# Kernel tuning notes

Hardware: AMD Instinct MI355X
Metric: run time of the kernel (lower is better)

Reference implementation:

```python
import jax, jax.numpy as jnp
import numpy as np

B, H, W, C = 16, 64, 64, 512
C2 = C // 2
LN_EPS = 1e-3  # Keras LayerNormalization default epsilon


def setup_inputs() -> dict:
    key = jax.random.key(0)
    ks = jax.random.split(key, 8)
    s = 0.02
    return {
        "x": jax.random.normal(ks[0], (B, H, W, C), dtype=jnp.float32),
        "ch_wv_w": jax.random.normal(ks[1], (C, C2), dtype=jnp.float32) * s,
        "ch_wv_b": jnp.zeros((C2,), jnp.float32),
        "ch_wq_w": jax.random.normal(ks[2], (C, 1), dtype=jnp.float32) * s,
        "ch_wq_b": jnp.zeros((1,), jnp.float32),
        "ch_wz_w": jax.random.normal(ks[3], (C2, C), dtype=jnp.float32) * s,
        "ch_wz_b": jnp.zeros((C,), jnp.float32),
        "ln_gamma": jnp.ones((C,), jnp.float32),
        "ln_beta": jnp.zeros((C,), jnp.float32),
        "sp_wv_w": jax.random.normal(ks[4], (C, C2), dtype=jnp.float32) * s,
        "sp_wv_b": jnp.zeros((C2,), jnp.float32),
        "sp_wq_w": jax.random.normal(ks[5], (C, C2), dtype=jnp.float32) * s,
        "sp_wq_b": jnp.zeros((C2,), jnp.float32),
    }


def reference(x, ch_wv_w, ch_wv_b, ch_wq_w, ch_wq_b, ch_wz_w, ch_wz_b,
              ln_gamma, ln_beta, sp_wv_w, sp_wv_b, sp_wq_w, sp_wq_b):
    b, h, w, c = x.shape
    n = h * w
    c2 = c // 2

    # ---- channel-only branch ----
    # 1x1 convs are pointwise GEMMs over the channel dim
    ch_wv = jnp.einsum('bhwc,cd->bhwd', x, ch_wv_w) + ch_wv_b      # (B,H,W,C/2)
    ch_wq = jnp.einsum('bhwc,co->bhwo', x, ch_wq_w) + ch_wq_b      # (B,H,W,1)
    ch_wv = ch_wv.reshape(b, n, c2)                                # (B,N,C/2)
    ch_wq = jax.nn.softmax(ch_wq.reshape(b, n, 1), axis=1)         # softmax over N
    ch_wz = jnp.einsum('bnd,bno->bd', ch_wv, ch_wq)                # (B,C/2)
    ch_wz = jnp.einsum('bd,dc->bc', ch_wz, ch_wz_w) + ch_wz_b      # (B,C)

    # LayerNorm over axes [1,2,3] of (B,1,1,C) == normalize over C
    mean = jnp.mean(ch_wz, axis=-1, keepdims=True)
    var = jnp.var(ch_wz, axis=-1, keepdims=True)
    ch_wz = (ch_wz - mean) * jax.lax.rsqrt(var + LN_EPS) * ln_gamma + ln_beta
    channel_weight = jax.nn.sigmoid(ch_wz)[:, None, None, :]       # (B,1,1,C)
    channel_out = channel_weight * x                               # (B,H,W,C)

    # ---- spatial-only branch ----
    sp_wv = jnp.einsum('bhwc,cd->bhwd', channel_out, sp_wv_w) + sp_wv_b  # (B,H,W,C/2)
    sp_wq = jnp.einsum('bhwc,cd->bhwd', channel_out, sp_wq_w) + sp_wq_b  # (B,H,W,C/2)
    sp_wq = jnp.mean(sp_wq, axis=(1, 2))                           # GAP -> (B,C/2)
    sp_wq = jax.nn.softmax(sp_wq, axis=-1)                         # softmax over C/2
    sp_wv = sp_wv.reshape(b, n, c2)                                # (B,N,C/2)
    sp_wz = jnp.einsum('bd,bnd->bn', sp_wq, sp_wv)                 # (B,N)
    spatial_weight = jax.nn.sigmoid(sp_wz).reshape(b, h, w, 1)     # (B,H,W,1)
    return spatial_weight * channel_out
```

## Files before the change

kernel.cpp:

```cpp
#include <hip/hip_runtime.h>
#include <math.h>

#define BB 16
#define NN 4096
#define CC 512
#define C2 256
#define CHUNKS 32
#define RPC (NN/CHUNKS)

__device__ __forceinline__ float sigmoidf_(float z){ return 1.0f/(1.0f + __expf(-z)); }
__device__ __forceinline__ float dot8_(float4 a0, float4 a1, float4 b0, float4 b1){
    return a0.x*b0.x + a0.y*b0.y + a0.z*b0.z + a0.w*b0.w
         + a1.x*b1.x + a1.y*b1.y + a1.z*b1.z + a1.w*b1.w;
}

__global__ __launch_bounds__(256) void k_stats(const float* __restrict__ x,
        const float* __restrict__ wq,
        float* __restrict__ part_w, float* __restrict__ part_g,
        float* __restrict__ chunk_m, float* __restrict__ chunk_d)
{
    const int b = blockIdx.x / CHUNKS;
    const int k = blockIdx.x % CHUNKS;
    const int tid = threadIdx.x, lane = tid & 63, wv = tid >> 6;
    __shared__ float s_log[RPC];
    __shared__ float s_e[RPC];
    __shared__ float g_part[4][CC];
    const long base = ((long)b*NN + (long)k*RPC) * CC;

    float4 w0 = *(const float4*)(wq + lane*4);
    float4 w1 = *(const float4*)(wq + 256 + lane*4);
    float g0x=0,g0y=0,g0z=0,g0w=0, g1x=0,g1y=0,g1z=0,g1w=0;

    for (int i = 0; i < RPC/4; ++i) {
        const int r = wv*(RPC/4) + i;
        const float* xr = x + base + (long)r*CC;
        float4 a0 = *(const float4*)(xr + lane*4);
        float4 a1 = *(const float4*)(xr + 256 + lane*4);
        float d = dot8_(a0, a1, w0, w1);
        #pragma unroll
        for (int off = 32; off; off >>= 1) d += __shfl_xor(d, off);
        if (lane == 0) s_log[r] = d;
        g0x+=a0.x; g0y+=a0.y; g0z+=a0.z; g0w+=a0.w;
        g1x+=a1.x; g1y+=a1.y; g1z+=a1.z; g1w+=a1.w;
    }
    g_part[wv][lane*4+0]=g0x; g_part[wv][lane*4+1]=g0y;
    g_part[wv][lane*4+2]=g0z; g_part[wv][lane*4+3]=g0w;
    g_part[wv][256+lane*4+0]=g1x; g_part[wv][256+lane*4+1]=g1y;
    g_part[wv][256+lane*4+2]=g1z; g_part[wv][256+lane*4+3]=g1w;
    __syncthreads();

    float m = -3.4e38f;
    #pragma unroll
    for (int r = 0; r < RPC; ++r) m = fmaxf(m, s_log[r]);
    if (tid < RPC) s_e[tid] = __expf(s_log[tid] - m);
    __syncthreads();
    if (tid == 0) {
        float dsum = 0.f;
        for (int r = 0; r < RPC; ++r) dsum += s_e[r];
        chunk_d[b*CHUNKS + k] = dsum;
        chunk_m[b*CHUNKS + k] = m;
    }

    const int c = 2*tid;
    float2 acc = {0.f, 0.f};
    for (int r = 0; r < RPC; ++r) {
        float2 v = *(const float2*)(x + base + (long)r*CC + c);
        float e = s_e[r];
        acc.x = fmaf(e, v.x, acc.x);
        acc.y = fmaf(e, v.y, acc.y);
    }
    *(float2*)(part_w + (long)(b*CHUNKS + k)*CC + c) = acc;
    float2 g;
    g.x = g_part[0][c]   + g_part[1][c]   + g_part[2][c]   + g_part[3][c];
    g.y = g_part[0][c+1] + g_part[1][c+1] + g_part[2][c+1] + g_part[3][c+1];
    *(float2*)(part_g + (long)(b*CHUNKS + k)*CC + c) = g;
}

__global__ __launch_bounds__(256) void k_combine(const float* __restrict__ part_w,
        const float* __restrict__ part_g,
        const float* __restrict__ chunk_m, const float* __restrict__ chunk_d,
        float* __restrict__ xbar, float* __restrict__ gapx)
{
    const int b  = blockIdx.x >> 3;
    const int cs = blockIdx.x & 7;
    const int tid = threadIdx.x, cl = tid & 63, q = tid >> 6;
    const int c = cs*64 + cl;
    __shared__ float s_scale[CHUNKS];
    __shared__ float s_w[4][64];
    __shared__ float s_g[4][64];
    const float* cm = chunk_m + b*CHUNKS;
    const float* cd = chunk_d + b*CHUNKS;
    float m = -3.4e38f;
    #pragma unroll
    for (int k = 0; k < CHUNKS; ++k) m = fmaxf(m, cm[k]);
    if (tid < CHUNKS) s_scale[tid] = __expf(cm[tid] - m);
    __syncthreads();
    float denom = 0.f;
    #pragma unroll
    for (int k = 0; k < CHUNKS; ++k) denom = fmaf(s_scale[k], cd[k], denom);
    float pw = 0.f, pg = 0.f;
    for (int k = q*8; k < q*8+8; ++k) {
        pw = fmaf(s_scale[k], part_w[(long)(b*CHUNKS + k)*CC + c], pw);
        pg += part_g[(long)(b*CHUNKS + k)*CC + c];
    }
    s_w[q][cl] = pw; s_g[q][cl] = pg;
    __syncthreads();
    if (q == 0) {
        float sw_ = s_w[0][cl]+s_w[1][cl]+s_w[2][cl]+s_w[3][cl];
        float sg_ = s_g[0][cl]+s_g[1][cl]+s_g[2][cl]+s_g[3][cl];
        xbar[b*CC + c] = sw_ / denom;
        gapx[b*CC + c] = sg_;
    }
}

__global__ __launch_bounds__(256) void k_gemv_cd(const float* __restrict__ vec,
        const float* __restrict__ W, const float* __restrict__ bias,
        float* __restrict__ out)
{
    const int bx = blockIdx.x;
    const int b  = blockIdx.y;
    const int tid = threadIdx.x, dl = tid & 63, q = tid >> 6;
    const int d = bx*64 + dl;
    __shared__ float s_x[CC];
    __shared__ float s_p[4][64];
    s_x[tid]       = vec[b*CC + tid];
    s_x[tid + 256] = vec[b*CC + tid + 256];
    __syncthreads();
    float a0=0,a1=0,a2=0,a3=0;
    #pragma unroll 8
    for (int c = q*128; c < q*128 + 128; c += 4) {
        a0 = fmaf(s_x[c+0], W[(c+0)*C2 + d], a0);
        a1 = fmaf(s_x[c+1], W[(c+1)*C2 + d], a1);
        a2 = fmaf(s_x[c+2], W[(c+2)*C2 + d], a2);
        a3 = fmaf(s_x[c+3], W[(c+3)*C2 + d], a3);
    }
    s_p[q][dl] = (a0+a1)+(a2+a3);
    __syncthreads();
    if (q == 0)
        out[b*C2 + d] = s_p[0][dl]+s_p[1][dl]+s_p[2][dl]+s_p[3][dl] + bias[d];
}

__global__ __launch_bounds__(256) void k_g2p(const float* __restrict__ mid,
        const float* __restrict__ Wz, float* __restrict__ part2)
{
    const int jd = blockIdx.x;
    const int b  = blockIdx.y;
    const int tid = threadIdx.x;
    __shared__ float s_m[32];
    if (tid < 32) s_m[tid] = mid[b*C2 + jd*32 + tid];
    __syncthreads();
    float a0 = 0.f, a1 = 0.f;
    #pragma unroll 8
    for (int dd = 0; dd < 32; ++dd) {
        const float mm = s_m[dd];
        const int d = jd*32 + dd;
        a0 = fmaf(mm, Wz[d*CC + tid],       a0);
        a1 = fmaf(mm, Wz[d*CC + tid + 256], a1);
    }
    part2[(long)(b*8 + jd)*CC + tid]       = a0;
    part2[(long)(b*8 + jd)*CC + tid + 256] = a1;
}

__global__ __launch_bounds__(256) void k_g2ln(const float* __restrict__ part2,
        const float* __restrict__ bz, const float* __restrict__ ln_g,
        const float* __restrict__ ln_b, const float* __restrict__ gapx,
        float* __restrict__ cw, float* __restrict__ gco)
{
    const int b = blockIdx.x, tid = threadIdx.x, lane = tid & 63, w = tid >> 6;
    __shared__ float s_red[8];
    float z0 = bz[tid], z1 = bz[tid + 256];
    #pragma unroll
    for (int jd = 0; jd < 8; ++jd) {
        z0 += part2[(long)(b*8 + jd)*CC + tid];
        z1 += part2[(long)(b*8 + jd)*CC + tid + 256];
    }
    float sum = z0 + z1, sq = z0*z0 + z1*z1;
    #pragma unroll
    for (int off = 32; off; off >>= 1) { sum += __shfl_xor(sum, off); sq += __shfl_xor(sq, off); }
    if (lane == 0) { s_red[w] = sum; s_red[4 + w] = sq; }
    __syncthreads();
    sum = s_red[0] + s_red[1] + s_red[2] + s_red[3];
    sq  = s_red[4] + s_red[5] + s_red[6] + s_red[7];
    const float mean = sum * (1.f/CC);
    const float var  = sq  * (1.f/CC) - mean*mean;
    const float rstd = rsqrtf(var + 1e-3f);
    float cw0 = sigmoidf_((z0 - mean)*rstd*ln_g[tid]       + ln_b[tid]);
    float cw1 = sigmoidf_((z1 - mean)*rstd*ln_g[tid + 256] + ln_b[tid + 256]);
    cw[b*CC + tid]       = cw0;
    cw[b*CC + tid + 256] = cw1;
    gco[b*CC + tid]       = cw0 * gapx[b*CC + tid]       * (1.f/NN);
    gco[b*CC + tid + 256] = cw1 * gapx[b*CC + tid + 256] * (1.f/NN);
}

__global__ __launch_bounds__(256) void k_g3sm(const float* __restrict__ qraw,
        const float* __restrict__ svb, float* __restrict__ qn, float* __restrict__ constb)
{
    const int b = blockIdx.x, tid = threadIdx.x, lane = tid & 63, w = tid >> 6;
    __shared__ float s_red[4];
    float v = qraw[b*C2 + tid];
    float mx = v;
    #pragma unroll
    for (int off = 32; off; off >>= 1) mx = fmaxf(mx, __shfl_xor(mx, off));
    if (lane == 0) s_red[w] = mx;
    __syncthreads();
    mx = fmaxf(fmaxf(s_red[0], s_red[1]), fmaxf(s_red[2], s_red[3]));
    __syncthreads();
    float e = __expf(v - mx);
    float se = e;
    #pragma unroll
    for (int off = 32; off; off >>= 1) se += __shfl_xor(se, off);
    if (lane == 0) s_red[w] = se;
    __syncthreads();
    se = s_red[0] + s_red[1] + s_red[2] + s_red[3];
    const float q = e / se;
    qn[b*C2 + tid] = q;
    float cb = q * svb[tid];
    #pragma unroll
    for (int off = 32; off; off >>= 1) cb += __shfl_xor(cb, off);
    __syncthreads();
    if (lane == 0) s_red[w] = cb;
    __syncthreads();
    if (tid == 0) constb[b] = s_red[0] + s_red[1] + s_red[2] + s_red[3];
}

__global__ __launch_bounds__(256) void k_veff(const float* __restrict__ Wv2,
        const float* __restrict__ qn, const float* __restrict__ cw,
        float* __restrict__ veff)
{
    const int lane = threadIdx.x & 63;
    const int wv   = threadIdx.x >> 6;
    const int gw = blockIdx.x*4 + wv;
    const int c = gw >> 4;
    const int b = gw & 15;
    float4 w4 = *(const float4*)(Wv2 + (long)c*C2 + lane*4);
    float4 q4 = *(const float4*)(qn + b*C2 + lane*4);
    float d = w4.x*q4.x + w4.y*q4.y + w4.z*q4.z + w4.w*q4.w;
    #pragma unroll
    for (int off = 32; off; off >>= 1) d += __shfl_xor(d, off);
    if (lane == 0) veff[b*CC + c] = cw[b*CC + c] * d;
}

__global__ __launch_bounds__(256) void k_final(const float* __restrict__ x,
        const float* __restrict__ cw, const float* __restrict__ veff,
        const float* __restrict__ constb, float* __restrict__ out)
{
    const int lane = threadIdx.x & 63;
    const int wv   = threadIdx.x >> 6;
    const long row = (long)blockIdx.x * 4 + wv;
    const int b = (int)(row >> 12);
    const float* xr = x + row * CC;
    float4 a0 = *(const float4*)(xr + lane*4);
    float4 a1 = *(const float4*)(xr + 256 + lane*4);
    const float* vb = veff + b*CC;
    float4 v0 = *(const float4*)(vb + lane*4);
    float4 v1 = *(const float4*)(vb + 256 + lane*4);
    float d = dot8_(a0, a1, v0, v1);
    #pragma unroll
    for (int off = 32; off; off >>= 1) d += __shfl_xor(d, off);
    const float sw = sigmoidf_(d + constb[b]);
    const float* cb = cw + b*CC;
    float4 c0 = *(const float4*)(cb + lane*4);
    float4 c1 = *(const float4*)(cb + 256 + lane*4);
    float4 o0, o1;
    o0.x = sw*c0.x*a0.x; o0.y = sw*c0.y*a0.y; o0.z = sw*c0.z*a0.z; o0.w = sw*c0.w*a0.w;
    o1.x = sw*c1.x*a1.x; o1.y = sw*c1.y*a1.y; o1.z = sw*c1.z*a1.z; o1.w = sw*c1.w*a1.w;
    *(float4*)(out + row*CC + lane*4)       = o0;
    *(float4*)(out + row*CC + 256 + lane*4) = o1;
}

extern "C" void kernel_launch(void* const* d_in, const int* in_sizes, int n_in,
                              void* d_out, int out_size, void* d_ws, size_t ws_size,
                              hipStream_t stream)
{
    const float* x       = (const float*)d_in[0];
    const float* ch_wv_w = (const float*)d_in[1];
    const float* ch_wv_b = (const float*)d_in[2];
    const float* ch_wq_w = (const float*)d_in[3];
    const float* ch_wz_w = (const float*)d_in[5];
    const float* ch_wz_b = (const float*)d_in[6];
    const float* ln_g    = (const float*)d_in[7];
    const float* ln_b    = (const float*)d_in[8];
    const float* sp_wv_w = (const float*)d_in[9];
    const float* sp_wv_b = (const float*)d_in[10];
    const float* sp_wq_w = (const float*)d_in[11];
    const float* sp_wq_b = (const float*)d_in[12];
    float* out = (float*)d_out;

    float* ws = (float*)d_ws;
    float* part_w  = ws;
    float* part_g  = part_w + BB*CHUNKS*CC;
    float* chunk_m = part_g + BB*CHUNKS*CC;
    float* chunk_d = chunk_m + BB*CHUNKS;
    float* xbar    = chunk_d + BB*CHUNKS;
    float* gapx    = xbar + BB*CC;
    float* mid     = gapx + BB*CC;
    float* part2   = mid + BB*C2;
    float* cw      = part2 + BB*8*CC;
    float* gco     = cw + BB*CC;
    float* qraw    = gco + BB*CC;
    float* qn      = qraw + BB*C2;
    float* constb  = qn + BB*C2;
    float* veff    = constb + BB;

    k_stats  <<<BB*CHUNKS, 256, 0, stream>>>(x, ch_wq_w, part_w, part_g, chunk_m, chunk_d);
    k_combine<<<BB*8,      256, 0, stream>>>(part_w, part_g, chunk_m, chunk_d, xbar, gapx);
    k_gemv_cd<<<dim3(4,BB),256, 0, stream>>>(xbar, ch_wv_w, ch_wv_b, mid);
    k_g2p    <<<dim3(8,BB),256, 0, stream>>>(mid, ch_wz_w, part2);
    k_g2ln   <<<BB,        256, 0, stream>>>(part2, ch_wz_b, ln_g, ln_b, gapx, cw, gco);
    k_gemv_cd<<<dim3(4,BB),256, 0, stream>>>(gco, sp_wq_w, sp_wq_b, qraw);
    k_g3sm   <<<BB,        256, 0, stream>>>(qraw, sp_wv_b, qn, constb);
    k_veff   <<<BB*CC/4,   256, 0, stream>>>(sp_wv_w, qn, cw, veff);
    k_final  <<<BB*NN/4,   256, 0, stream>>>(x, cw, veff, constb, out);
}
```

Before: 107.0 us.

## Fuse small mid-stage kernels into one flag-synchronized persistent kernel

Replaces seven small launches (combine, two GEMVs, Wz projection, LayerNorm, softmax, veff) with a single kernel. Block ranges handle the stages and hand off per batch through atomic counters with acquire/release spin-waits. The aim is to remove launch gaps and the serialization between tiny kernels. It also doubles the stats chunk count for more parallelism and switches the per-chunk softmax to wave shuffles. It relies on all 592 blocks being co-resident, or on blocks being scheduled in order, to avoid deadlock; a guard counter caps the spin so a stall cannot hang forever.

```diff
diff --git a/kernel.cpp b/kernel.cpp
--- a/kernel.cpp
+++ b/kernel.cpp
@@ -5,7 +5,7 @@
 #define NN 4096
 #define CC 512
 #define C2 256
-#define CHUNKS 32
+#define CHUNKS 64
 #define RPC (NN/CHUNKS)
 
 __device__ __forceinline__ float sigmoidf_(float z){ return 1.0f/(1.0f + __expf(-z)); }
@@ -14,10 +14,27 @@
          + a1.x*b1.x + a1.y*b1.y + a1.z*b1.z + a1.w*b1.w;
 }
 
+__device__ __forceinline__ void sig_add(int* f) {
+    __syncthreads();
+    if (threadIdx.x == 0)
+        __hip_atomic_fetch_add(f, 1, __ATOMIC_RELEASE, __HIP_MEMORY_SCOPE_AGENT);
+}
+__device__ __forceinline__ void wait_ge(int* f, int target) {
+    if (threadIdx.x == 0) {
+        int guard = 0;
+        while (__hip_atomic_load(f, __ATOMIC_ACQUIRE, __HIP_MEMORY_SCOPE_AGENT) < target) {
+            __builtin_amdgcn_s_sleep(8);
+            if (++guard > (1 << 22)) break;
+        }
+    }
+    __syncthreads();
+}
+
 __global__ __launch_bounds__(256) void k_stats(const float* __restrict__ x,
         const float* __restrict__ wq,
         float* __restrict__ part_w, float* __restrict__ part_g,
-        float* __restrict__ chunk_m, float* __restrict__ chunk_d)
+        float* __restrict__ chunk_m, float* __restrict__ chunk_d,
+        int* __restrict__ flags)
 {
     const int b = blockIdx.x / CHUNKS;
     const int k = blockIdx.x % CHUNKS;
@@ -25,8 +42,9 @@
     __shared__ float s_log[RPC];
     __shared__ float s_e[RPC];
     __shared__ float g_part[4][CC];
+    if (blockIdx.x == 0 && tid < 128) flags[tid] = 0;
+
     const long base = ((long)b*NN + (long)k*RPC) * CC;
-
     float4 w0 = *(const float4*)(wq + lane*4);
     float4 w1 = *(const float4*)(wq + 256 + lane*4);
     float g0x=0,g0y=0,g0z=0,g0w=0, g1x=0,g1y=0,g1z=0,g1w=0;
@@ -49,17 +67,19 @@
     g_part[wv][256+lane*4+2]=g1z; g_part[wv][256+lane*4+3]=g1w;
     __syncthreads();
 
-    float m = -3.4e38f;
-    #pragma unroll
-    for (int r = 0; r < RPC; ++r) m = fmaxf(m, s_log[r]);
-    if (tid < RPC) s_e[tid] = __expf(s_log[tid] - m);
+    if (tid < 64) {
+        float mk = s_log[tid];
+        float m = mk;
+        #pragma unroll
+        for (int off = 32; off; off >>= 1) m = fmaxf(m, __shfl_xor(m, off));
+        float e = __expf(mk - m);
+        s_e[tid] = e;
+        float ds = e;
+        #pragma unroll
+        for (int off = 32; off; off >>= 1) ds += __shfl_xor(ds, off);
+        if (tid == 0) { chunk_m[b*CHUNKS + k] = m; chunk_d[b*CHUNKS + k] = ds; }
+    }
     __syncthreads();
-    if (tid == 0) {
-        float dsum = 0.f;
-        for (int r = 0; r < RPC; ++r) dsum += s_e[r];
-        chunk_d[b*CHUNKS + k] = dsum;
-        chunk_m[b*CHUNKS + k] = m;
-    }
 
     const int c = 2*tid;
     float2 acc = {0.f, 0.f};
@@ -76,168 +96,206 @@
     *(float2*)(part_g + (long)(b*CHUNKS + k)*CC + c) = g;
 }
 
-__global__ __launch_bounds__(256) void k_combine(const float* __restrict__ part_w,
-        const float* __restrict__ part_g,
-        const float* __restrict__ chunk_m, const float* __restrict__ chunk_d,
-        float* __restrict__ xbar, float* __restrict__ gapx)
+__global__ __launch_bounds__(256, 4) void k_mid(
+    const float* __restrict__ part_w, const float* __restrict__ part_g,
+    const float* __restrict__ chunk_m, const float* __restrict__ chunk_d,
+    const float* __restrict__ Wv,  const float* __restrict__ bv,
+    const float* __restrict__ Wz,  const float* __restrict__ bz,
+    const float* __restrict__ lng, const float* __restrict__ lnb,
+    const float* __restrict__ Wq,  const float* __restrict__ bq,
+    const float* __restrict__ Wv2, const float* __restrict__ bv2,
+    float* __restrict__ xbar, float* __restrict__ gapx,
+    float* __restrict__ mid,  float* __restrict__ part2,
+    float* __restrict__ cw,   float* __restrict__ gco,
+    float* __restrict__ qraw, float* __restrict__ veff, float* __restrict__ constb,
+    int* __restrict__ flags)
 {
-    const int b  = blockIdx.x >> 3;
-    const int cs = blockIdx.x & 7;
-    const int tid = threadIdx.x, cl = tid & 63, q = tid >> 6;
-    const int c = cs*64 + cl;
-    __shared__ float s_scale[CHUNKS];
-    __shared__ float s_w[4][64];
-    __shared__ float s_g[4][64];
-    const float* cm = chunk_m + b*CHUNKS;
-    const float* cd = chunk_d + b*CHUNKS;
-    float m = -3.4e38f;
-    #pragma unroll
-    for (int k = 0; k < CHUNKS; ++k) m = fmaxf(m, cm[k]);
-    if (tid < CHUNKS) s_scale[tid] = __expf(cm[tid] - m);
-    __syncthreads();
-    float denom = 0.f;
-    #pragma unroll
-    for (int k = 0; k < CHUNKS; ++k) denom = fmaf(s_scale[k], cd[k], denom);
-    float pw = 0.f, pg = 0.f;
-    for (int k = q*8; k < q*8+8; ++k) {
-        pw = fmaf(s_scale[k], part_w[(long)(b*CHUNKS + k)*CC + c], pw);
-        pg += part_g[(long)(b*CHUNKS + k)*CC + c];
-    }
-    s_w[q][cl] = pw; s_g[q][cl] = pg;
-    __syncthreads();
-    if (q == 0) {
-        float sw_ = s_w[0][cl]+s_w[1][cl]+s_w[2][cl]+s_w[3][cl];
-        float sg_ = s_g[0][cl]+s_g[1][cl]+s_g[2][cl]+s_g[3][cl];
-        xbar[b*CC + c] = sw_ / denom;
-        gapx[b*CC + c] = sg_;
-    }
-}
-
-__global__ __launch_bounds__(256) void k_gemv_cd(const float* __restrict__ vec,
-        const float* __restrict__ W, const float* __restrict__ bias,
-        float* __restrict__ out)
-{
-    const int bx = blockIdx.x;
-    const int b  = blockIdx.y;
-    const int tid = threadIdx.x, dl = tid & 63, q = tid >> 6;
-    const int d = bx*64 + dl;
-    __shared__ float s_x[CC];
-    __shared__ float s_p[4][64];
-    s_x[tid]       = vec[b*CC + tid];
-    s_x[tid + 256] = vec[b*CC + tid + 256];
-    __syncthreads();
-    float a0=0,a1=0,a2=0,a3=0;
-    #pragma unroll 8
-    for (int c = q*128; c < q*128 + 128; c += 4) {
-        a0 = fmaf(s_x[c+0], W[(c+0)*C2 + d], a0);
-        a1 = fmaf(s_x[c+1], W[(c+1)*C2 + d], a1);
-        a2 = fmaf(s_x[c+2], W[(c+2)*C2 + d], a2);
-        a3 = fmaf(s_x[c+3], W[(c+3)*C2 + d], a3);
-    }
-    s_p[q][dl] = (a0+a1)+(a2+a3);
-    __syncthreads();
-    if (q == 0)
-        out[b*C2 + d] = s_p[0][dl]+s_p[1][dl]+s_p[2][dl]+s_p[3][dl] + bias[d];
-}
-
-__global__ __launch_bounds__(256) void k_g2p(const float* __restrict__ mid,
-        const float* __restrict__ Wz, float* __restrict__ part2)
-{
-    const int jd = blockIdx.x;
-    const int b  = blockIdx.y;
-    const int tid = threadIdx.x;
-    __shared__ float s_m[32];
-    if (tid < 32) s_m[tid] = mid[b*C2 + jd*32 + tid];
-    __syncthreads();
-    float a0 = 0.f, a1 = 0.f;
-    #pragma unroll 8
-    for (int dd = 0; dd < 32; ++dd) {
-        const float mm = s_m[dd];
-        const int d = jd*32 + dd;
-        a0 = fmaf(mm, Wz[d*CC + tid],       a0);
-        a1 = fmaf(mm, Wz[d*CC + tid + 256], a1);
-    }
-    part2[(long)(b*8 + jd)*CC + tid]       = a0;
-    part2[(long)(b*8 + jd)*CC + tid + 256] = a1;
-}
-
-__global__ __launch_bounds__(256) void k_g2ln(const float* __restrict__ part2,
-        const float* __restrict__ bz, const float* __restrict__ ln_g,
-        const float* __restrict__ ln_b, const float* __restrict__ gapx,
-        float* __restrict__ cw, float* __restrict__ gco)
-{
-    const int b = blockIdx.x, tid = threadIdx.x, lane = tid & 63, w = tid >> 6;
-    __shared__ float s_red[8];
-    float z0 = bz[tid], z1 = bz[tid + 256];
-    #pragma unroll
-    for (int jd = 0; jd < 8; ++jd) {
-        z0 += part2[(long)(b*8 + jd)*CC + tid];
-        z1 += part2[(long)(b*8 + jd)*CC + tid + 256];
-    }
-    float sum = z0 + z1, sq = z0*z0 + z1*z1;
-    #pragma unroll
-    for (int off = 32; off; off >>= 1) { sum += __shfl_xor(sum, off); sq += __shfl_xor(sq, off); }
-    if (lane == 0) { s_red[w] = sum; s_red[4 + w] = sq; }
-    __syncthreads();
-    sum = s_red[0] + s_red[1] + s_red[2] + s_red[3];
-    sq  = s_red[4] + s_red[5] + s_red[6] + s_red[7];
-    const float mean = sum * (1.f/CC);
-    const float var  = sq  * (1.f/CC) - mean*mean;
-    const float rstd = rsqrtf(var + 1e-3f);
-    float cw0 = sigmoidf_((z0 - mean)*rstd*ln_g[tid]       + ln_b[tid]);
-    float cw1 = sigmoidf_((z1 - mean)*rstd*ln_g[tid + 256] + ln_b[tid + 256]);
-    cw[b*CC + tid]       = cw0;
-    cw[b*CC + tid + 256] = cw1;
-    gco[b*CC + tid]       = cw0 * gapx[b*CC + tid]       * (1.f/NN);
-    gco[b*CC + tid + 256] = cw1 * gapx[b*CC + tid + 256] * (1.f/NN);
-}
-
-__global__ __launch_bounds__(256) void k_g3sm(const float* __restrict__ qraw,
-        const float* __restrict__ svb, float* __restrict__ qn, float* __restrict__ constb)
-{
-    const int b = blockIdx.x, tid = threadIdx.x, lane = tid & 63, w = tid >> 6;
-    __shared__ float s_red[4];
-    float v = qraw[b*C2 + tid];
-    float mx = v;
-    #pragma unroll
-    for (int off = 32; off; off >>= 1) mx = fmaxf(mx, __shfl_xor(mx, off));
-    if (lane == 0) s_red[w] = mx;
-    __syncthreads();
-    mx = fmaxf(fmaxf(s_red[0], s_red[1]), fmaxf(s_red[2], s_red[3]));
-    __syncthreads();
-    float e = __expf(v - mx);
-    float se = e;
-    #pragma unroll
-    for (int off = 32; off; off >>= 1) se += __shfl_xor(se, off);
-    if (lane == 0) s_red[w] = se;
-    __syncthreads();
-    se = s_red[0] + s_red[1] + s_red[2] + s_red[3];
-    const float q = e / se;
-    qn[b*C2 + tid] = q;
-    float cb = q * svb[tid];
-    #pragma unroll
-    for (int off = 32; off; off >>= 1) cb += __shfl_xor(cb, off);
-    __syncthreads();
-    if (lane == 0) s_red[w] = cb;
-    __syncthreads();
-    if (tid == 0) constb[b] = s_red[0] + s_red[1] + s_red[2] + s_red[3];
-}
-
-__global__ __launch_bounds__(256) void k_veff(const float* __restrict__ Wv2,
-        const float* __restrict__ qn, const float* __restrict__ cw,
-        float* __restrict__ veff)
-{
-    const int lane = threadIdx.x & 63;
-    const int wv   = threadIdx.x >> 6;
-    const int gw = blockIdx.x*4 + wv;
-    const int c = gw >> 4;
-    const int b = gw & 15;
-    float4 w4 = *(const float4*)(Wv2 + (long)c*C2 + lane*4);
-    float4 q4 = *(const float4*)(qn + b*C2 + lane*4);
-    float d = w4.x*q4.x + w4.y*q4.y + w4.z*q4.z + w4.w*q4.w;
-    #pragma unroll
-    for (int off = 32; off; off >>= 1) d += __shfl_xor(d, off);
-    if (lane == 0) veff[b*CC + c] = cw[b*CC + c] * d;
+    __shared__ float4 sm4[576];
+    float* sm = (float*)sm4;
+    int* f0 = flags;
+    int* f1 = flags + 16;
+    int* f2 = flags + 32;
+    int* f3 = flags + 48;
+    int* f4 = flags + 64;
+    const int blk = blockIdx.x, tid = threadIdx.x;
+    const int lane = tid & 63, w = tid >> 6;
+
+    if (blk < 64) {
+        const int b = blk >> 2, c0 = (blk & 3) * 128;
+        if (tid < 64) {
+            float mk = chunk_m[b*CHUNKS + tid];
+            float m = mk;
+            #pragma unroll
+            for (int off = 32; off; off >>= 1) m = fmaxf(m, __shfl_xor(m, off));
+            float e = __expf(mk - m);
+            float dn = e * chunk_d[b*CHUNKS + tid];
+            #pragma unroll
+            for (int off = 32; off; off >>= 1) dn += __shfl_xor(dn, off);
+            sm[tid] = e;
+            if (tid == 0) sm[64] = dn;
+        }
+        __syncthreads();
+        const int cl = tid & 127, kh = tid >> 7;
+        float pw = 0.f, pg = 0.f;
+        for (int kk = 0; kk < 32; ++kk) {
+            const int k = kh*32 + kk;
+            const float s = sm[k];
+            pw = fmaf(s, part_w[(long)(b*CHUNKS + k)*CC + c0 + cl], pw);
+            pg +=      part_g[(long)(b*CHUNKS + k)*CC + c0 + cl];
+        }
+        sm[128 + kh*128 + cl] = pw;
+        sm[384 + kh*128 + cl] = pg;
+        __syncthreads();
+        if (tid < 128) {
+            const float inv = 1.f / sm[64];
+            xbar[b*CC + c0 + tid] = (sm[128+tid] + sm[256+tid]) * inv;
+            gapx[b*CC + c0 + tid] =  sm[384+tid] + sm[512+tid];
+        }
+        sig_add(&f0[b]);
+    }
+    else if (blk < 192) {
+        const int i = blk - 64, b = i >> 3, d0 = (i & 7) * 32;
+        wait_ge(&f0[b], 4);
+        sm[tid]       = xbar[b*CC + tid];
+        sm[256 + tid] = xbar[b*CC + 256 + tid];
+        __syncthreads();
+        const int dl = tid & 31, cg = tid >> 5;
+        float acc = 0.f;
+        #pragma unroll 4
+        for (int cc = 0; cc < 64; ++cc) {
+            const int cidx = cg*64 + cc;
+            acc = fmaf(sm[cidx], Wv[(long)cidx*C2 + d0 + dl], acc);
+        }
+        sm[512 + cg*32 + dl] = acc;
+        __syncthreads();
+        if (tid < 32) {
+            float s = 0.f;
+            #pragma unroll
+            for (int g = 0; g < 8; ++g) s += sm[512 + g*32 + tid];
+            mid[b*C2 + d0 + tid] = s + bv[d0 + tid];
+        }
+        sig_add(&f1[b]);
+    }
+    else if (blk < 320) {
+        const int i = blk - 192, b = i >> 3, jd = i & 7;
+        wait_ge(&f1[b], 8);
+        if (tid < 32) sm[tid] = mid[b*C2 + jd*32 + tid];
+        __syncthreads();
+        const int c4 = tid & 127, dh = tid >> 7;
+        const float4* Wz4 = (const float4*)Wz;
+        float4 a = {0.f,0.f,0.f,0.f};
+        #pragma unroll 4
+        for (int ii = 0; ii < 16; ++ii) {
+            const int dd = dh*16 + ii;
+            const float mval = sm[dd];
+            const float4 wr = Wz4[(long)(jd*32 + dd)*128 + c4];
+            a.x = fmaf(mval, wr.x, a.x); a.y = fmaf(mval, wr.y, a.y);
+            a.z = fmaf(mval, wr.z, a.z); a.w = fmaf(mval, wr.w, a.w);
+        }
+        float4* smp = sm4 + 16;
+        smp[dh*128 + c4] = a;
+        __syncthreads();
+        if (tid < 128) {
+            const float4 r0 = smp[tid], r1 = smp[128 + tid];
+            float4 o = {r0.x+r1.x, r0.y+r1.y, r0.z+r1.z, r0.w+r1.w};
+            ((float4*)part2)[(long)(b*8 + jd)*128 + tid] = o;
+        }
+        sig_add(&f2[b]);
+    }
+    else if (blk < 336) {
+        const int b = blk - 320;
+        wait_ge(&f2[b], 8);
+        float z0 = bz[tid], z1 = bz[tid + 256];
+        #pragma unroll
+        for (int jd = 0; jd < 8; ++jd) {
+            z0 += part2[(long)(b*8 + jd)*CC + tid];
+            z1 += part2[(long)(b*8 + jd)*CC + tid + 256];
+        }
+        float sum = z0 + z1, sq = z0*z0 + z1*z1;
+        #pragma unroll
+        for (int off = 32; off; off >>= 1) { sum += __shfl_xor(sum, off); sq += __shfl_xor(sq, off); }
+        if (lane == 0) { sm[w] = sum; sm[4 + w] = sq; }
+        __syncthreads();
+        sum = sm[0] + sm[1] + sm[2] + sm[3];
+        sq  = sm[4] + sm[5] + sm[6] + sm[7];
+        const float mean = sum * (1.f/CC);
+        const float var  = sq  * (1.f/CC) - mean*mean;
+        const float rstd = rsqrtf(var + 1e-3f);
+        const float cw0 = sigmoidf_((z0 - mean)*rstd*lng[tid]       + lnb[tid]);
+        const float cw1 = sigmoidf_((z1 - mean)*rstd*lng[tid + 256] + lnb[tid + 256]);
+        cw[b*CC + tid]       = cw0;
+        cw[b*CC + tid + 256] = cw1;
+        gco[b*CC + tid]       = cw0 * gapx[b*CC + tid]       * (1.f/NN);
+        gco[b*CC + tid + 256] = cw1 * gapx[b*CC + tid + 256] * (1.f/NN);
+        sig_add(&f3[b]);
+    }
+    else if (blk < 464) {
+        const int i = blk - 336, b = i >> 3, d0 = (i & 7) * 32;
+        wait_ge(&f3[b], 1);
+        sm[tid]       = gco[b*CC + tid];
+        sm[256 + tid] = gco[b*CC + 256 + tid];
+        __syncthreads();
+        const int dl = tid & 31, cg = tid >> 5;
+        float acc = 0.f;
+        #pragma unroll 4
+        for (int cc = 0; cc < 64; ++cc) {
+            const int cidx = cg*64 + cc;
+            acc = fmaf(sm[cidx], Wq[(long)cidx*C2 + d0 + dl], acc);
+        }
+        sm[512 + cg*32 + dl] = acc;
+        __syncthreads();
+        if (tid < 32) {
+            float s = 0.f;
+            #pragma unroll
+            for (int g = 0; g < 8; ++g) s += sm[512 + g*32 + tid];
+            qraw[b*C2 + d0 + tid] = s + bq[d0 + tid];
+        }
+        sig_add(&f4[b]);
+    }
+    else {
+        const int i = blk - 464, b = i >> 3, c0 = (i & 7) * 64;
+        wait_ge(&f4[b], 8);
+        const float v = qraw[b*C2 + tid];
+        float mx = v;
+        #pragma unroll
+        for (int off = 32; off; off >>= 1) mx = fmaxf(mx, __shfl_xor(mx, off));
+        if (lane == 0) sm[tid >> 6] = mx;
+        __syncthreads();
+        mx = fmaxf(fmaxf(sm[0], sm[1]), fmaxf(sm[2], sm[3]));
+        __syncthreads();
+        const float e = __expf(v - mx);
+        float se = e;
+        #pragma unroll
+        for (int off = 32; off; off >>= 1) se += __shfl_xor(se, off);
+        if (lane == 0) sm[4 + w] = se;
+        __syncthreads();
+        se = sm[4] + sm[5] + sm[6] + sm[7];
+        const float qv = e / se;
+        sm[8 + tid] = qv;
+        float cb = qv * bv2[tid];
+        #pragma unroll
+        for (int off = 32; off; off >>= 1) cb += __shfl_xor(cb, off);
+        if (lane == 0) sm[264 + w] = cb;
+        __syncthreads();
+        if (tid == 0 && (i & 7) == 0)
+            constb[b] = sm[264] + sm[265] + sm[266] + sm[267];
+        const int dg = tid & 3, cl = tid >> 2;
+        const int cidx = c0 + cl;
+        const float4* W4  = (const float4*)Wv2;
+        const float4* qn4 = (const float4*)(sm + 8);
+        float acc = 0.f;
+        #pragma unroll 4
+        for (int ii = 0; ii < 16; ++ii) {
+            const float4 wv4 = W4[(long)cidx*64 + dg*16 + ii];
+            const float4 q4  = qn4[dg*16 + ii];
+            acc += wv4.x*q4.x + wv4.y*q4.y + wv4.z*q4.z + wv4.w*q4.w;
+        }
+        sm[300 + cl*4 + dg] = acc;
+        __syncthreads();
+        if (tid < 64)
+            veff[b*CC + c0 + tid] = cw[b*CC + c0 + tid] *
+                (sm[300+tid*4] + sm[300+tid*4+1] + sm[300+tid*4+2] + sm[300+tid*4+3]);
+    }
 }
 
 __global__ __launch_bounds__(256) void k_final(const float* __restrict__ x,
@@ -298,17 +356,15 @@
     float* cw      = part2 + BB*8*CC;
     float* gco     = cw + BB*CC;
     float* qraw    = gco + BB*CC;
-    float* qn      = qraw + BB*C2;
-    float* constb  = qn + BB*C2;
-    float* veff    = constb + BB;
-
-    k_stats  <<<BB*CHUNKS, 256, 0, stream>>>(x, ch_wq_w, part_w, part_g, chunk_m, chunk_d);
-    k_combine<<<BB*8,      256, 0, stream>>>(part_w, part_g, chunk_m, chunk_d, xbar, gapx);
-    k_gemv_cd<<<dim3(4,BB),256, 0, stream>>>(xbar, ch_wv_w, ch_wv_b, mid);
-    k_g2p    <<<dim3(8,BB),256, 0, stream>>>(mid, ch_wz_w, part2);
-    k_g2ln   <<<BB,        256, 0, stream>>>(part2, ch_wz_b, ln_g, ln_b, gapx, cw, gco);
-    k_gemv_cd<<<dim3(4,BB),256, 0, stream>>>(gco, sp_wq_w, sp_wq_b, qraw);
-    k_g3sm   <<<BB,        256, 0, stream>>>(qraw, sp_wv_b, qn, constb);
-    k_veff   <<<BB*CC/4,   256, 0, stream>>>(sp_wv_w, qn, cw, veff);
-    k_final  <<<BB*NN/4,   256, 0, stream>>>(x, cw, veff, constb, out);
-}
+    float* veff    = qraw + BB*C2;
+    float* constb  = veff + BB*CC;
+    int*   flags   = (int*)(constb + BB);
+
+    k_stats<<<BB*CHUNKS, 256, 0, stream>>>(x, ch_wq_w, part_w, part_g, chunk_m, chunk_d, flags);
+    k_mid  <<<592,       256, 0, stream>>>(part_w, part_g, chunk_m, chunk_d,
+                                           ch_wv_w, ch_wv_b, ch_wz_w, ch_wz_b,
+                                           ln_g, ln_b, sp_wq_w, sp_wq_b, sp_wv_w, sp_wv_b,
+                                           xbar, gapx, mid, part2, cw, gco, qraw, veff, constb,
+                                           flags);
+    k_final<<<BB*NN/4,   256, 0, stream>>>(x, cw, veff, constb, out);
+}
```

Result: slower. 221.1 us (+106.5%).
